# Optimization experiments

Hardware: AMD Instinct MI355X
Metric: run time of the kernel (lower is better)

Reference implementation:

```python
import jax, jax.numpy as jnp
import numpy as np

B, S, H, I, E, TOP_K = 2, 1024, 1024, 2048, 8, 2


def setup_inputs() -> dict:
    key = jax.random.key(0)
    k1, k2, k3, k4 = jax.random.split(key, 4)
    return {
        "hidden_states": jax.random.normal(k1, (B, S, H), dtype=jnp.float32),
        "gate_weight": jax.random.normal(k2, (E, H), dtype=jnp.float32) * 0.02,
        "gate_up_proj": jax.random.normal(k3, (E, 2 * I, H), dtype=jnp.float32) * 0.02,
        "down_proj": jax.random.normal(k4, (E, H, I), dtype=jnp.float32) * 0.02,
    }


def reference(hidden_states, gate_weight, gate_up_proj, down_proj):
    b, s, h = hidden_states.shape
    T = b * s
    x = hidden_states.reshape(T, h)

    # --- router ---
    router_logits = x @ gate_weight.T                          # [T, E]
    router_probs = jax.nn.softmax(router_logits.astype(jnp.float32), axis=-1)
    router_probs = router_probs.astype(router_logits.dtype)
    top_vals, top_idx = jax.lax.top_k(router_probs, TOP_K)     # [T, K]
    # norm_topk_prob = True
    routing_weights = top_vals / jnp.maximum(top_vals.sum(-1, keepdims=True), 1e-12)

    # --- dense all-expert FFN ---
    gu = jnp.einsum('th,eoh->eto', x, gate_up_proj)            # [E, T, 2I]
    gate_h, up_h = jnp.split(gu, 2, axis=-1)
    inter = jax.nn.silu(gate_h) * up_h                          # [E, T, I]
    expert_out = jnp.einsum('eti,ehi->eth', inter, down_proj).astype(jnp.float32)  # [E, T, H]

    # --- pairwise Frobenius similarity (sim = 1 - dist/max_dist, diag=1) ---
    flat = expert_out.reshape(E, -1)
    gram = flat @ flat.T                                        # [E, E]
    sq = jnp.diagonal(gram)
    dist = jnp.sqrt(jnp.clip(sq[:, None] + sq[None, :] - 2.0 * gram, 0.0))
    dist = dist.at[jnp.arange(E), jnp.arange(E)].set(0.0)
    sim = 1.0 - dist / jnp.maximum(dist.max(), 1e-12)
    sim = sim.at[jnp.arange(E), jnp.arange(E)].set(1.0)

    # --- top-k weighted combine (gather along expert axis) ---
    gathered = expert_out[top_idx, jnp.arange(T)[:, None]]      # [T, K, H]
    final = (gathered * routing_weights[..., None].astype(jnp.float32)).sum(axis=1)
    final = final.astype(hidden_states.dtype).reshape(b, s, h)
    return final, sim
```

## Files before the change

### kernel.cpp

```cpp
#include <hip/hip_runtime.h>
#include <math.h>

#define T_TOK 2048
#define H_DIM 1024
#define I_DIM 2048
#define NEXP  8

typedef _Float16 f16x8 __attribute__((ext_vector_type(8)));
typedef _Float16 f16x4 __attribute__((ext_vector_type(4)));
typedef float    f32x4 __attribute__((ext_vector_type(4)));

__device__ __forceinline__ void cp16(const void* g, void* l) {
  __builtin_amdgcn_global_load_lds(
      (const __attribute__((address_space(1))) void*)g,
      (__attribute__((address_space(3))) void*)l, 16, 0, 0);
}

__global__ __launch_bounds__(256) void cvt_f16_kernel(
    const float* __restrict__ in, _Float16* __restrict__ hi, int n) {
  int i = (blockIdx.x * 256 + threadIdx.x) * 4;
  if (i >= n) return;
  float4 v = *(const float4*)(in + i);
  f16x4 hv = {(_Float16)v.x, (_Float16)v.y, (_Float16)v.z, (_Float16)v.w};
  *(f16x4*)(hi + i) = hv;
}

__global__ __launch_bounds__(256) void prep_kernel(
    const float* __restrict__ x, _Float16* __restrict__ xHi,
    const float* __restrict__ gup, _Float16* __restrict__ gup16,
    const float* __restrict__ dwn, _Float16* __restrict__ wd16,
    const float* __restrict__ gw,
    int* __restrict__ topIdx, float* __restrict__ topW,
    float* __restrict__ gram) {
  const int b = blockIdx.x;
  const int tid = threadIdx.x;

  if (b < 512) {
    if (b == 0 && tid < 36) gram[tid] = 0.f;
    const int wave = tid >> 6, lane = tid & 63;
    const int t = b * 4 + wave;
    float p[NEXP];
#pragma unroll
    for (int e = 0; e < NEXP; ++e) p[e] = 0.f;
    const float* xr = x + (size_t)t * H_DIM;
    for (int h = lane; h < H_DIM; h += 64) {
      float xv = xr[h];
#pragma unroll
      for (int e = 0; e < NEXP; ++e) p[e] += xv * gw[e * H_DIM + h];
    }
#pragma unroll
    for (int e = 0; e < NEXP; ++e) {
      float v = p[e];
      for (int off = 32; off > 0; off >>= 1) v += __shfl_down(v, off);
      p[e] = v;
    }
    if (lane == 0) {
      float mx = p[0];
#pragma unroll
      for (int e = 1; e < NEXP; ++e) mx = fmaxf(mx, p[e]);
      float ex[NEXP], s = 0.f;
#pragma unroll
      for (int e = 0; e < NEXP; ++e) { ex[e] = expf(p[e] - mx); s += ex[e]; }
#pragma unroll
      for (int e = 0; e < NEXP; ++e) ex[e] /= s;
      int i0 = 0; float v0 = ex[0];
#pragma unroll
      for (int e = 1; e < NEXP; ++e) if (ex[e] > v0) { v0 = ex[e]; i0 = e; }
      int i1 = -1; float v1 = -1.f;
#pragma unroll
      for (int e = 0; e < NEXP; ++e) if (e != i0 && ex[e] > v1) { v1 = ex[e]; i1 = e; }
      float sum = fmaxf(v0 + v1, 1e-12f);
      topIdx[2 * t] = i0;  topIdx[2 * t + 1] = i1;
      topW[2 * t] = v0 / sum;  topW[2 * t + 1] = v1 / sum;
    }
    return;
  }

  int rb = b - 512;
  const float* src;
  _Float16* dst;
  if (rb < 2048) {
    src = x;  dst = xHi;
  } else if (rb < 2048 + 32768) {
    rb -= 2048;  src = gup;  dst = gup16;
  } else {
    rb -= (2048 + 32768);  src = dwn;  dst = wd16;
  }
  const size_t i = (size_t)rb * 1024 + (size_t)tid * 4;
  float4 v = *(const float4*)(src + i);
  f16x4 hv = {(_Float16)v.x, (_Float16)v.y, (_Float16)v.z, (_Float16)v.w};
  *(f16x4*)(dst + i) = hv;
}

__global__ __launch_bounds__(256, 2) void gemm_gateup(
    const _Float16* __restrict__ xHi, const _Float16* __restrict__ gup16,
    _Float16* __restrict__ intHi) {
  __shared__ _Float16 lds[24576];

  const int tid = threadIdx.x;
  const int wave = tid >> 6, lane = tid & 63;
  const int rowA0 = blockIdx.y * 128;
  const int colB0 = blockIdx.x * 128;
  const int e = blockIdx.z;

  const int sr = lane >> 3;
  const int sc = lane & 7;
  const int gcol = (sc ^ sr) * 8;
  const int rbase = wave * 8 + sr;

  const int wm = wave >> 1, wn = wave & 1;
  const int fr = lane & 15;
  const int quad = lane >> 4;

  f32x4 accG[4][4], accU[4][4];
#pragma unroll
  for (int i = 0; i < 4; ++i)
#pragma unroll
    for (int j = 0; j < 4; ++j) {
      accG[i][j] = (f32x4){0.f, 0.f, 0.f, 0.f};
      accU[i][j] = (f32x4){0.f, 0.f, 0.f, 0.f};
    }

  const _Float16* gupG = gup16 + ((size_t)e * 2 * I_DIM + colB0) * H_DIM;
  const _Float16* gupU = gupG + (size_t)I_DIM * H_DIM;
  char* ldsB = (char*)lds;

  for (int k0 = 0; k0 < H_DIM; k0 += 64) {
    const int kcol = k0 + gcol;
#pragma unroll
    for (int i = 0; i < 4; ++i) {
      const int row = i * 32 + rbase;
      const unsigned dst = (unsigned)(i * 4096 + wave * 1024);
      cp16(xHi  + (size_t)(rowA0 + row) * H_DIM + kcol, ldsB + dst);
      cp16(gupG + (size_t)row * H_DIM + kcol, ldsB + 16384u + dst);
      cp16(gupU + (size_t)row * H_DIM + kcol, ldsB + 32768u + dst);
    }
    __syncthreads();

#pragma unroll
    for (int kk = 0; kk < 2; ++kk) {
      f16x8 ah[4];
#pragma unroll
      for (int i = 0; i < 4; ++i) {
        const int row = wm * 64 + i * 16 + fr;
        ah[i] = *(const f16x8*)&lds[row * 64 + (((kk * 4 + quad) ^ (fr & 7)) * 8)];
      }
#pragma unroll
      for (int j = 0; j < 4; ++j) {
        const int row = wn * 64 + j * 16 + fr;
        const int boff = row * 64 + (((kk * 4 + quad) ^ (fr & 7)) * 8);
        f16x8 bg = *(const f16x8*)&lds[8192 + boff];
        f16x8 bu = *(const f16x8*)&lds[16384 + boff];
#pragma unroll
        for (int i = 0; i < 4; ++i) {
          accG[i][j] = __builtin_amdgcn_mfma_f32_16x16x32_f16(ah[i], bg, accG[i][j], 0, 0, 0);
          accU[i][j] = __builtin_amdgcn_mfma_f32_16x16x32_f16(ah[i], bu, accU[i][j], 0, 0, 0);
        }
      }
    }
    __syncthreads();
  }

  const int er = quad * 4;
  const int ec = lane & 15;
#pragma unroll
  for (int i = 0; i < 4; ++i)
#pragma unroll
    for (int j = 0; j < 4; ++j) {
      const int row = rowA0 + wm * 64 + i * 16 + er;
      const int col = colB0 + wn * 64 + j * 16 + ec;
#pragma unroll
      for (int r = 0; r < 4; ++r) {
        float g = accG[i][j][r], u = accU[i][j][r];
        float val = g / (1.f + __expf(-g)) * u;
        intHi[((size_t)e * T_TOK + row + r) * I_DIM + col] = (_Float16)val;
      }
    }
}

__global__ __launch_bounds__(512, 4) void gemm_down(
    const _Float16* __restrict__ intHi, const _Float16* __restrict__ wd16,
    _Float16* __restrict__ eo) {
  __shared__ _Float16 lds[24576];

  const int tid = threadIdx.x;
  const int wave = tid >> 6, lane = tid & 63;
  const int rowA0 = blockIdx.x * 128;
  const int colB0 = blockIdx.y * 256;
  const int e = blockIdx.z;

  const int sr = lane >> 3;
  const int sc = lane & 7;
  const int gcol = (sc ^ sr) * 8;

  const int wm = wave >> 2;
  const int wn = wave & 3;
  const int fr = lane & 15;
  const int quad = lane >> 4;

  f32x4 acc[4][4];
#pragma unroll
  for (int i = 0; i < 4; ++i)
#pragma unroll
    for (int j = 0; j < 4; ++j) acc[i][j] = (f32x4){0.f, 0.f, 0.f, 0.f};

  const _Float16* aSrc = intHi + (size_t)e * T_TOK * I_DIM +
                         (size_t)(rowA0 + wave * 8 + sr) * I_DIM + gcol;
  const _Float16* bSrc = wd16 + ((size_t)e * H_DIM + colB0 + wave * 8 + sr) * I_DIM + gcol;
  char* ldsB = (char*)lds;

  for (int k0 = 0; k0 < I_DIM; k0 += 64) {
#pragma unroll
    for (int c = 0; c < 2; ++c)
      cp16(aSrc + (size_t)c * 64 * I_DIM + k0, ldsB + c * 8192u + wave * 1024u);
#pragma unroll
    for (int c = 0; c < 4; ++c)
      cp16(bSrc + (size_t)c * 64 * I_DIM + k0, ldsB + 16384u + c * 8192u + wave * 1024u);
    __syncthreads();

#pragma unroll
    for (int kk = 0; kk < 2; ++kk) {
      const int ksl = kk * 4 + quad;
      f16x8 ah[4];
#pragma unroll
      for (int i = 0; i < 4; ++i) {
        const int row = wm * 64 + i * 16 + fr;
        ah[i] = *(const f16x8*)&lds[row * 64 + ((ksl ^ (fr & 7)) * 8)];
      }
#pragma unroll
      for (int j = 0; j < 4; ++j) {
        const int row = wn * 64 + j * 16 + fr;
        f16x8 bh = *(const f16x8*)&lds[8192 + row * 64 + ((ksl ^ (fr & 7)) * 8)];
#pragma unroll
        for (int i = 0; i < 4; ++i)
          acc[i][j] = __builtin_amdgcn_mfma_f32_16x16x32_f16(ah[i], bh, acc[i][j], 0, 0, 0);
      }
    }
    __syncthreads();
  }

  const int er = quad * 4;
  const int ec = lane & 15;
#pragma unroll
  for (int i = 0; i < 4; ++i)
#pragma unroll
    for (int j = 0; j < 4; ++j) {
      const int row = rowA0 + wm * 64 + i * 16 + er;
      const int col = colB0 + wn * 64 + j * 16 + ec;
#pragma unroll
      for (int r = 0; r < 4; ++r)
        eo[((size_t)e * T_TOK + row + r) * H_DIM + col] = (_Float16)acc[i][j][r];
    }
}

__global__ __launch_bounds__(256) void gram_kernel(
    const _Float16* __restrict__ eo, float* __restrict__ gram) {
  float s[36];
#pragma unroll
  for (int p = 0; p < 36; ++p) s[p] = 0.f;
  const size_t total = (size_t)T_TOK * H_DIM;
  const size_t stride = (size_t)gridDim.x * 256 * 8;
  for (size_t j = ((size_t)blockIdx.x * 256 + threadIdx.x) * 8; j < total; j += stride) {
    f16x8 ve[NEXP];
#pragma unroll
    for (int e = 0; e < NEXP; ++e) ve[e] = *(const f16x8*)&eo[(size_t)e * total + j];
#pragma unroll
    for (int k = 0; k < 8; ++k) {
      float v[NEXP];
#pragma unroll
      for (int e = 0; e < NEXP; ++e) v[e] = (float)ve[e][k];
      int p = 0;
#pragma unroll
      for (int a = 0; a < NEXP; ++a)
#pragma unroll
        for (int b = a; b < NEXP; ++b) { s[p] += v[a] * v[b]; ++p; }
    }
  }
#pragma unroll
  for (int p = 0; p < 36; ++p) {
    float v = s[p];
    for (int off = 32; off > 0; off >>= 1) v += __shfl_down(v, off);
    s[p] = v;
  }
  __shared__ float red[4][36];
  const int wave = threadIdx.x >> 6, lane = threadIdx.x & 63;
  if (lane == 0)
#pragma unroll
    for (int p = 0; p < 36; ++p) red[wave][p] = s[p];
  __syncthreads();
  if (threadIdx.x < 36) {
    float v = red[0][threadIdx.x] + red[1][threadIdx.x] + red[2][threadIdx.x] + red[3][threadIdx.x];
    atomicAdd(&gram[threadIdx.x], v);
  }
}

__global__ __launch_bounds__(256) void final_kernel(
    const _Float16* __restrict__ eo, const int* __restrict__ topIdx,
    const float* __restrict__ topW, const float* __restrict__ gram,
    float* __restrict__ out) {
  const int t = blockIdx.x;
  if (t == T_TOK) {
    if (threadIdx.x < 64) {
      const int q = threadIdx.x;
      const int e1 = q >> 3, e2 = q & 7;
      int a = e1 < e2 ? e1 : e2;
      int b = e1 < e2 ? e2 : e1;
      const float g = gram[a * 8 - a * (a - 1) / 2 + (b - a)];
      const float sq1 = gram[e1 * 8 - e1 * (e1 - 1) / 2];
      const float sq2 = gram[e2 * 8 - e2 * (e2 - 1) / 2];
      float d2 = fmaxf(sq1 + sq2 - 2.f * g, 0.f);
      float dist = (e1 == e2) ? 0.f : sqrtf(d2);
      float dmax = dist;
      for (int off = 32; off > 0; off >>= 1) dmax = fmaxf(dmax, __shfl_xor(dmax, off));
      float sim = 1.f - dist / fmaxf(dmax, 1e-12f);
      if (e1 == e2) sim = 1.f;
      out[(size_t)T_TOK * H_DIM + q] = sim;
    }
    return;
  }
  const int c = threadIdx.x * 4;
  const int i0 = topIdx[2 * t], i1 = topIdx[2 * t + 1];
  const float w0 = topW[2 * t], w1 = topW[2 * t + 1];
  const size_t per = (size_t)T_TOK * H_DIM;
  f16x4 a = *(const f16x4*)&eo[(size_t)i0 * per + (size_t)t * H_DIM + c];
  f16x4 b = *(const f16x4*)&eo[(size_t)i1 * per + (size_t)t * H_DIM + c];
  float4 r;
  r.x = w0 * (float)a[0] + w1 * (float)b[0];
  r.y = w0 * (float)a[1] + w1 * (float)b[1];
  r.z = w0 * (float)a[2] + w1 * (float)b[2];
  r.w = w0 * (float)a[3] + w1 * (float)b[3];
  *(float4*)&out[(size_t)t * H_DIM + c] = r;
}

extern "C" void kernel_launch(void* const* d_in, const int* in_sizes, int n_in,
                              void* d_out, int out_size, void* d_ws, size_t ws_size,
                              hipStream_t stream) {
  (void)in_sizes; (void)n_in; (void)out_size;
  const float* x   = (const float*)d_in[0];
  const float* gw  = (const float*)d_in[1];
  const float* gup = (const float*)d_in[2];
  const float* dwn = (const float*)d_in[3];
  float* out = (float*)d_out;

  char* ws = (char*)d_ws;
  const size_t MB = 1u << 20;
  _Float16* xHi    = (_Float16*)(ws + 0 * MB);
  _Float16* intHi  = (_Float16*)(ws + 4 * MB);
  _Float16* gup16  = (_Float16*)(ws + 68 * MB);
  _Float16* eo     = (_Float16*)(ws + 100 * MB);
  int*      topIdx = (int*)(ws + 132 * MB);
  float*    topW   = (float*)(ws + 132 * MB + 16384);
  float*    gram   = (float*)(ws + 132 * MB + 32768);

  const int doDwn = ws_size >= (size_t)169 * MB;
  _Float16* wd16 = doDwn ? (_Float16*)(ws + 136 * MB)
                         : (_Float16*)(ws + 68 * MB);

  const int prepBlocks = 512 + 2048 + 32768 + (doDwn ? 16384 : 0);
  prep_kernel<<<prepBlocks, 256, 0, stream>>>(
      x, xHi, gup, gup16, dwn, wd16, gw, topIdx, topW, gram);

  gemm_gateup<<<dim3(I_DIM / 128, T_TOK / 128, NEXP), 256, 0, stream>>>(
      xHi, gup16, intHi);

  if (!doDwn)
    cvt_f16_kernel<<<16384, 256, 0, stream>>>(dwn, wd16, NEXP * H_DIM * I_DIM);

  gemm_down<<<dim3(T_TOK / 128, H_DIM / 256, NEXP), 512, 0, stream>>>(
      intHi, wd16, eo);

  gram_kernel<<<1024, 256, 0, stream>>>(eo, gram);
  final_kernel<<<T_TOK + 1, 256, 0, stream>>>(eo, topIdx, topW, gram, out);
}
```

Baseline: 491.3 us.

## Add three-stage async LDS pipeline to both FFN GEMMs and widen gate-up blocks

Both expert GEMMs now use a triple-buffered LDS pipeline. Tiles are prefetched three k-steps ahead with global_load_lds, and explicit vmcnt waits and barriers replace the load-sync-compute-sync loop. The gate/up kernel moves to 512 threads, each wave computing a 4x4 tile in which gate and up columns are interleaved in the B tile, rather than separate gate and up accumulators. The goal is to hide global load latency behind MFMA work, at the cost of 144KB LDS per block, which limits occupancy (down kernel launch bounds reduced to 2 blocks).

```diff
diff --git a/kernel.cpp b/kernel.cpp
--- a/kernel.cpp
+++ b/kernel.cpp
@@ -15,6 +15,10 @@
       (const __attribute__((address_space(1))) void*)g,
       (__attribute__((address_space(3))) void*)l, 16, 0, 0);
 }
+
+#define WAITV(N) asm volatile("s_waitcnt vmcnt(" #N ")" ::: "memory")
+#define SB0() __builtin_amdgcn_sched_barrier(0)
+#define BAR() __builtin_amdgcn_s_barrier()
 
 __global__ __launch_bounds__(256) void cvt_f16_kernel(
     const float* __restrict__ in, _Float16* __restrict__ hi, int n) {
@@ -92,96 +96,114 @@
   *(f16x4*)(dst + i) = hv;
 }
 
-__global__ __launch_bounds__(256, 2) void gemm_gateup(
+__global__ __launch_bounds__(512, 2) void gemm_gateup(
     const _Float16* __restrict__ xHi, const _Float16* __restrict__ gup16,
     _Float16* __restrict__ intHi) {
-  __shared__ _Float16 lds[24576];
+  __shared__ _Float16 lds[73728];
 
   const int tid = threadIdx.x;
   const int wave = tid >> 6, lane = tid & 63;
+  const int colB0 = blockIdx.x * 128;
   const int rowA0 = blockIdx.y * 128;
-  const int colB0 = blockIdx.x * 128;
   const int e = blockIdx.z;
 
   const int sr = lane >> 3;
   const int sc = lane & 7;
   const int gcol = (sc ^ sr) * 8;
-  const int rbase = wave * 8 + sr;
-
-  const int wm = wave >> 1, wn = wave & 1;
+
+  const int wm = wave >> 2;
+  const int wn = wave & 3;
   const int fr = lane & 15;
   const int quad = lane >> 4;
 
-  f32x4 accG[4][4], accU[4][4];
+  f32x4 acc[4][4];
 #pragma unroll
   for (int i = 0; i < 4; ++i)
 #pragma unroll
-    for (int j = 0; j < 4; ++j) {
-      accG[i][j] = (f32x4){0.f, 0.f, 0.f, 0.f};
-      accU[i][j] = (f32x4){0.f, 0.f, 0.f, 0.f};
-    }
-
-  const _Float16* gupG = gup16 + ((size_t)e * 2 * I_DIM + colB0) * H_DIM;
-  const _Float16* gupU = gupG + (size_t)I_DIM * H_DIM;
+    for (int j = 0; j < 4; ++j) acc[i][j] = (f32x4){0.f, 0.f, 0.f, 0.f};
+
+  const _Float16* aSrc = xHi + (size_t)(rowA0 + wave * 8 + sr) * H_DIM + gcol;
+  const _Float16* bSrc = gup16 +
+      ((size_t)e * 2 * I_DIM + (size_t)(wave >> 2) * I_DIM + colB0 +
+       (wave & 3) * 8 + sr) * H_DIM + gcol;
   char* ldsB = (char*)lds;
-
-  for (int k0 = 0; k0 < H_DIM; k0 += 64) {
-    const int kcol = k0 + gcol;
-#pragma unroll
-    for (int i = 0; i < 4; ++i) {
-      const int row = i * 32 + rbase;
-      const unsigned dst = (unsigned)(i * 4096 + wave * 1024);
-      cp16(xHi  + (size_t)(rowA0 + row) * H_DIM + kcol, ldsB + dst);
-      cp16(gupG + (size_t)row * H_DIM + kcol, ldsB + 16384u + dst);
-      cp16(gupU + (size_t)row * H_DIM + kcol, ldsB + 32768u + dst);
-    }
-    __syncthreads();
-
+  const unsigned wb = wave * 1024u;
+
+  auto STAGE = [&](unsigned bufByte, int kt) {
+    const int k0 = kt * 64;
+#pragma unroll
+    for (int c = 0; c < 2; ++c)
+      cp16(aSrc + (size_t)c * 64 * H_DIM + k0, ldsB + bufByte + c * 8192u + wb);
+#pragma unroll
+    for (int c = 0; c < 4; ++c)
+      cp16(bSrc + (size_t)c * 32 * H_DIM + k0,
+           ldsB + bufByte + 16384u + c * 8192u + wb);
+  };
+
+  auto COMPUTE = [&](int bufElem) {
 #pragma unroll
     for (int kk = 0; kk < 2; ++kk) {
+      const int ksl = kk * 4 + quad;
       f16x8 ah[4];
 #pragma unroll
       for (int i = 0; i < 4; ++i) {
         const int row = wm * 64 + i * 16 + fr;
-        ah[i] = *(const f16x8*)&lds[row * 64 + (((kk * 4 + quad) ^ (fr & 7)) * 8)];
+        ah[i] = *(const f16x8*)&lds[bufElem + row * 64 + ((ksl ^ (fr & 7)) * 8)];
       }
 #pragma unroll
       for (int j = 0; j < 4; ++j) {
         const int row = wn * 64 + j * 16 + fr;
-        const int boff = row * 64 + (((kk * 4 + quad) ^ (fr & 7)) * 8);
-        f16x8 bg = *(const f16x8*)&lds[8192 + boff];
-        f16x8 bu = *(const f16x8*)&lds[16384 + boff];
-#pragma unroll
-        for (int i = 0; i < 4; ++i) {
-          accG[i][j] = __builtin_amdgcn_mfma_f32_16x16x32_f16(ah[i], bg, accG[i][j], 0, 0, 0);
-          accU[i][j] = __builtin_amdgcn_mfma_f32_16x16x32_f16(ah[i], bu, accU[i][j], 0, 0, 0);
-        }
+        f16x8 bh = *(const f16x8*)&lds[bufElem + 8192 + row * 64 + ((ksl ^ (fr & 7)) * 8)];
+#pragma unroll
+        for (int i = 0; i < 4; ++i)
+          acc[i][j] = __builtin_amdgcn_mfma_f32_16x16x32_f16(ah[i], bh, acc[i][j], 0, 0, 0);
       }
     }
-    __syncthreads();
-  }
+  };
+
+  const int NT = H_DIM / 64;
+  STAGE(0u, 0);
+  STAGE(49152u, 1);
+  STAGE(98304u, 2);
+
+  int cur = 0;
+  for (int t = 0; t < NT - 2; ++t) {
+    WAITV(12); SB0();
+    BAR(); SB0();
+    COMPUTE(cur * 24576);
+    SB0(); BAR(); SB0();
+    if (t + 3 < NT) STAGE((unsigned)cur * 49152u, t + 3);
+    cur = (cur == 2) ? 0 : cur + 1;
+  }
+  WAITV(6); SB0();
+  BAR(); SB0();
+  COMPUTE(cur * 24576);
+  cur = (cur == 2) ? 0 : cur + 1;
+  WAITV(0); SB0();
+  BAR(); SB0();
+  COMPUTE(cur * 24576);
 
   const int er = quad * 4;
   const int ec = lane & 15;
 #pragma unroll
   for (int i = 0; i < 4; ++i)
 #pragma unroll
-    for (int j = 0; j < 4; ++j) {
+    for (int jj = 0; jj < 2; ++jj) {
       const int row = rowA0 + wm * 64 + i * 16 + er;
-      const int col = colB0 + wn * 64 + j * 16 + ec;
+      const int col = colB0 + wn * 32 + jj * 16 + ec;
 #pragma unroll
       for (int r = 0; r < 4; ++r) {
-        float g = accG[i][j][r], u = accU[i][j][r];
+        float g = acc[i][jj][r], u = acc[i][jj + 2][r];
         float val = g / (1.f + __expf(-g)) * u;
         intHi[((size_t)e * T_TOK + row + r) * I_DIM + col] = (_Float16)val;
       }
     }
 }
 
-__global__ __launch_bounds__(512, 4) void gemm_down(
+__global__ __launch_bounds__(512, 2) void gemm_down(
     const _Float16* __restrict__ intHi, const _Float16* __restrict__ wd16,
     _Float16* __restrict__ eo) {
-  __shared__ _Float16 lds[24576];
+  __shared__ _Float16 lds[73728];
 
   const int tid = threadIdx.x;
   const int wave = tid >> 6, lane = tid & 63;
@@ -206,18 +228,23 @@
 
   const _Float16* aSrc = intHi + (size_t)e * T_TOK * I_DIM +
                          (size_t)(rowA0 + wave * 8 + sr) * I_DIM + gcol;
-  const _Float16* bSrc = wd16 + ((size_t)e * H_DIM + colB0 + wave * 8 + sr) * I_DIM + gcol;
+  const _Float16* bSrc = wd16 +
+      ((size_t)e * H_DIM + colB0 + wave * 8 + sr) * I_DIM + gcol;
   char* ldsB = (char*)lds;
-
-  for (int k0 = 0; k0 < I_DIM; k0 += 64) {
+  const unsigned wb = wave * 1024u;
+
+  auto STAGE = [&](unsigned bufByte, int kt) {
+    const int k0 = kt * 64;
 #pragma unroll
     for (int c = 0; c < 2; ++c)
-      cp16(aSrc + (size_t)c * 64 * I_DIM + k0, ldsB + c * 8192u + wave * 1024u);
+      cp16(aSrc + (size_t)c * 64 * I_DIM + k0, ldsB + bufByte + c * 8192u + wb);
 #pragma unroll
     for (int c = 0; c < 4; ++c)
-      cp16(bSrc + (size_t)c * 64 * I_DIM + k0, ldsB + 16384u + c * 8192u + wave * 1024u);
-    __syncthreads();
-
+      cp16(bSrc + (size_t)c * 64 * I_DIM + k0,
+           ldsB + bufByte + 16384u + c * 8192u + wb);
+  };
+
+  auto COMPUTE = [&](int bufElem) {
 #pragma unroll
     for (int kk = 0; kk < 2; ++kk) {
       const int ksl = kk * 4 + quad;
@@ -225,19 +252,40 @@
 #pragma unroll
       for (int i = 0; i < 4; ++i) {
         const int row = wm * 64 + i * 16 + fr;
-        ah[i] = *(const f16x8*)&lds[row * 64 + ((ksl ^ (fr & 7)) * 8)];
+        ah[i] = *(const f16x8*)&lds[bufElem + row * 64 + ((ksl ^ (fr & 7)) * 8)];
       }
 #pragma unroll
       for (int j = 0; j < 4; ++j) {
         const int row = wn * 64 + j * 16 + fr;
-        f16x8 bh = *(const f16x8*)&lds[8192 + row * 64 + ((ksl ^ (fr & 7)) * 8)];
+        f16x8 bh = *(const f16x8*)&lds[bufElem + 8192 + row * 64 + ((ksl ^ (fr & 7)) * 8)];
 #pragma unroll
         for (int i = 0; i < 4; ++i)
           acc[i][j] = __builtin_amdgcn_mfma_f32_16x16x32_f16(ah[i], bh, acc[i][j], 0, 0, 0);
       }
     }
-    __syncthreads();
-  }
+  };
+
+  const int NT = I_DIM / 64;
+  STAGE(0u, 0);
+  STAGE(49152u, 1);
+  STAGE(98304u, 2);
+
+  int cur = 0;
+  for (int t = 0; t < NT - 2; ++t) {
+    WAITV(12); SB0();
+    BAR(); SB0();
+    COMPUTE(cur * 24576);
+    SB0(); BAR(); SB0();
+    if (t + 3 < NT) STAGE((unsigned)cur * 49152u, t + 3);
+    cur = (cur == 2) ? 0 : cur + 1;
+  }
+  WAITV(6); SB0();
+  BAR(); SB0();
+  COMPUTE(cur * 24576);
+  cur = (cur == 2) ? 0 : cur + 1;
+  WAITV(0); SB0();
+  BAR(); SB0();
+  COMPUTE(cur * 24576);
 
   const int er = quad * 4;
   const int ec = lane & 15;
@@ -360,7 +408,7 @@
   prep_kernel<<<prepBlocks, 256, 0, stream>>>(
       x, xHi, gup, gup16, dwn, wd16, gw, topIdx, topW, gram);
 
-  gemm_gateup<<<dim3(I_DIM / 128, T_TOK / 128, NEXP), 256, 0, stream>>>(
+  gemm_gateup<<<dim3(I_DIM / 128, T_TOK / 128, NEXP), 512, 0, stream>>>(
       xHi, gup16, intHi);
 
   if (!doDwn)
```

Measured after the change: 514.2 us. 4.7% more time.
